# Optimization experiments

Measured on AMD Instinct MI355X. Metric: run time of the kernel, lower is better.

## Reference

```python
import jax, jax.numpy as jnp
import numpy as np

INPUT_SIZE = 512
HIDDEN_SIZE = 1024
SEQ_LEN = 512
BATCH = 64


def _xavier(key, shape):
    fan_out, fan_in = shape
    limit = float(np.sqrt(6.0 / (fan_in + fan_out)))
    return jax.random.uniform(key, shape, jnp.float32, -limit, limit)


def setup_inputs() -> dict:
    key = jax.random.key(0)
    ks = jax.random.split(key, 10)
    return {
        "x_seq": jax.random.normal(ks[0], (SEQ_LEN, BATCH, INPUT_SIZE), jnp.float32),
        "h": jax.random.normal(ks[1], (BATCH, HIDDEN_SIZE), jnp.float32),
        "U_c": _xavier(ks[2], (HIDDEN_SIZE, INPUT_SIZE)),
        "w_c": jax.random.normal(ks[3], (HIDDEN_SIZE,), jnp.float32),
        "b_c": jax.random.normal(ks[4], (HIDDEN_SIZE,), jnp.float32),
        "U_a": _xavier(ks[5], (HIDDEN_SIZE, INPUT_SIZE)),
        "w_a": jax.random.normal(ks[6], (HIDDEN_SIZE,), jnp.float32),
        "b_a": jax.random.normal(ks[7], (HIDDEN_SIZE,), jnp.float32),
        "U_h": _xavier(ks[8], (HIDDEN_SIZE, INPUT_SIZE)),
        "b_h": jax.random.normal(ks[9], (HIDDEN_SIZE,), jnp.float32),
    }


def reference(x_seq, h, U_c, w_c, b_c, U_a, w_a, b_a, U_h, b_h):
    # Precompute all input projections in one big batched GEMM each:
    # (S, B, I) @ (I, H) -> (S, B, H)
    xc = jnp.einsum("sbi,hi->sbh", x_seq, U_c) + b_c
    xa = jnp.einsum("sbi,hi->sbh", x_seq, U_a) + b_a
    xh = jnp.einsum("sbi,hi->sbh", x_seq, U_h) + b_h

    def step(h, proj):
        pc, pa, ph = proj
        c = jax.nn.sigmoid(pc + w_c * h)
        a = 1.0 + jnp.tanh(pa + w_a * h)
        h_new = c * h + (1.0 - c) * jnp.tanh(ph + a * h)
        return h_new, h_new

    hn, y_seq = jax.lax.scan(step, h, (xc, xa, xh))
    return y_seq, hn
```

## Files before the change

### kernel.cpp

```cpp
#include <hip/hip_runtime.h>
#include <hip/hip_bf16.h>
#include <stdint.h>

#define SEQLEN 512
#define NBATCH 64
#define KDIM   512
#define HDIM   1024
#define MTOT   (SEQLEN * NBATCH)
#define NTOT   (3 * HDIM)
#define STRIDE (NBATCH * HDIM)

typedef __attribute__((ext_vector_type(4))) float f32x4;
typedef _Float16 f16x8 __attribute__((ext_vector_type(8)));

__global__ __launch_bounds__(256) void cvt_x(const float* __restrict__ x,
                                             _Float16* __restrict__ xh,
                                             _Float16* __restrict__ xl) {
    int i = blockIdx.x * 256 + threadIdx.x;
    const float4* s = (const float4*)(x + (size_t)i * 8);
    float4 a = s[0], b = s[1];
    float v[8] = {a.x, a.y, a.z, a.w, b.x, b.y, b.z, b.w};
    f16x8 hi, lo;
#pragma unroll
    for (int j = 0; j < 8; ++j) {
        _Float16 h = (_Float16)v[j];
        hi[j] = h;
        lo[j] = (_Float16)(v[j] - (float)h);
    }
    *(f16x8*)(xh + (size_t)i * 8) = hi;
    *(f16x8*)(xl + (size_t)i * 8) = lo;
}

__global__ __launch_bounds__(256) void cvt_u(const float* __restrict__ Uc,
                                             const float* __restrict__ Ua,
                                             const float* __restrict__ Uh,
                                             _Float16* __restrict__ uh,
                                             _Float16* __restrict__ ul) {
    int i = blockIdx.x * 256 + threadIdx.x;
    int n = i >> 6;
    int kb = (i & 63) * 8;
    const float* src = (n < HDIM) ? (Uc + (size_t)n * KDIM)
                     : (n < 2 * HDIM) ? (Ua + (size_t)(n - HDIM) * KDIM)
                     : (Uh + (size_t)(n - 2 * HDIM) * KDIM);
    const float4* s = (const float4*)(src + kb);
    float4 a = s[0], b = s[1];
    float v[8] = {a.x, a.y, a.z, a.w, b.x, b.y, b.z, b.w};
    f16x8 hi, lo;
#pragma unroll
    for (int j = 0; j < 8; ++j) {
        _Float16 h = (_Float16)v[j];
        hi[j] = h;
        lo[j] = (_Float16)(v[j] - (float)h);
    }
    *(f16x8*)(uh + (size_t)n * KDIM + kb) = hi;
    *(f16x8*)(ul + (size_t)n * KDIM + kb) = lo;
}

#define BM 256
#define BN 256
#define BK 32
#define NT_N (NTOT / BN)
#define GRID ((MTOT / BM) * NT_N)
#define KT_N (KDIM / BK)

__device__ __forceinline__ void gload16(const _Float16* g, _Float16* l) {
    __builtin_amdgcn_global_load_lds((const __attribute__((address_space(1))) void*)g,
                                     (__attribute__((address_space(3))) void*)l,
                                     16, 0, 0);
}

__device__ __forceinline__ f32x4 mfma16(f16x8 a, f16x8 b, f32x4 c) {
    return __builtin_amdgcn_mfma_f32_16x16x32_f16(a, b, c, 0, 0, 0);
}

__global__ __launch_bounds__(512, 2) void gemm_f16x2(const _Float16* __restrict__ Ah,
                                                     const _Float16* __restrict__ Al,
                                                     const _Float16* __restrict__ Bh,
                                                     const _Float16* __restrict__ Bl,
                                                     float* __restrict__ pc,
                                                     float* __restrict__ pa,
                                                     float* __restrict__ ph) {
    __shared__ _Float16 lds[2][4][BM * BK];

    int bid  = blockIdx.x;
    int bm   = bid / NT_N;
    int bn   = bid % NT_N;
    int tid  = threadIdx.x;
    int lane = tid & 63;
    int wave = tid >> 6;
    int wr   = wave >> 2;
    int wc   = wave & 3;

    size_t row_off = (size_t)(tid >> 2) * KDIM
                   + (size_t)(((tid & 3) ^ ((tid >> 3) & 3)) * 8);
    const _Float16* gAh = Ah + (size_t)bm * BM * KDIM + row_off;
    const _Float16* gAl = Al + (size_t)bm * BM * KDIM + row_off;
    const _Float16* gBh = Bh + (size_t)bn * BN * KDIM + row_off;
    const _Float16* gBl = Bl + (size_t)bn * BN * KDIM + row_off;
    const size_t HPAN = (size_t)128 * KDIM;
    int t8 = tid * 8;

#define SPAIR(buf, plane, gp, kt) do { int _g = (kt) * BK;                     \
    gload16((gp) + _g,        &lds[buf][plane][t8]);                           \
    gload16((gp) + HPAN + _g, &lds[buf][plane][t8 + 4096]); } while (0)

    f32x4 acc[8][4];
#pragma unroll
    for (int i = 0; i < 8; ++i)
#pragma unroll
        for (int j = 0; j < 4; ++j)
            acc[i][j] = (f32x4){0.f, 0.f, 0.f, 0.f};

    int ro = lane & 15;
    int ko = ((lane >> 4) ^ ((lane >> 1) & 3)) * 8;

    f16x8 a_[4][2], b_[4][2];

#define READ_A(mh) _Pragma("unroll")                                           \
    for (int i = 0; i < 4; ++i) {                                              \
        int row = wr * 128 + ((mh) * 4 + i) * 16 + ro;                         \
        a_[i][0] = *(const f16x8*)(&lds[cur][0][row * BK + ko]);               \
        a_[i][1] = *(const f16x8*)(&lds[cur][1][row * BK + ko]);               \
    }
#define READ_B() _Pragma("unroll")                                             \
    for (int j = 0; j < 4; ++j) {                                              \
        int row = wc * 64 + j * 16 + ro;                                       \
        b_[j][0] = *(const f16x8*)(&lds[cur][2][row * BK + ko]);               \
        b_[j][1] = *(const f16x8*)(&lds[cur][3][row * BK + ko]);               \
    }
#define MFMA_HALF(mh) _Pragma("unroll")                                        \
    for (int i = 0; i < 4; ++i) _Pragma("unroll")                              \
        for (int j = 0; j < 4; ++j) {                                          \
            f32x4 c = acc[(mh) * 4 + i][j];                                    \
            c = mfma16(a_[i][0], b_[j][1], c);                      \
            c = mfma16(a_[i][1], b_[j][0], c);                      \
            c = mfma16(a_[i][0], b_[j][0], c);                      \
            acc[(mh) * 4 + i][j] = c;                                          \
        }

    SPAIR(0, 0, gAh, 0);
    SPAIR(0, 1, gAl, 0);
    SPAIR(0, 2, gBh, 0);
    SPAIR(0, 3, gBl, 0);

    for (int kt = 0; kt < KT_N; ++kt) {
        int cur = kt & 1, nxt = 1 - cur;
        bool pre = (kt < KT_N - 1);
        __builtin_amdgcn_sched_barrier(0);
        asm volatile("s_waitcnt vmcnt(0)" ::: "memory");
        __builtin_amdgcn_s_barrier();
        __builtin_amdgcn_sched_barrier(0);

        READ_B();
        READ_A(0);
        if (pre) { SPAIR(nxt, 0, gAh, kt + 1); SPAIR(nxt, 1, gAl, kt + 1); }
        __builtin_amdgcn_s_setprio(1);
        MFMA_HALF(0);
        __builtin_amdgcn_s_setprio(0);
        READ_A(1);
        if (pre) { SPAIR(nxt, 2, gBh, kt + 1); SPAIR(nxt, 3, gBl, kt + 1); }
        __builtin_amdgcn_s_setprio(1);
        MFMA_HALF(1);
        __builtin_amdgcn_s_setprio(0);
    }

    int n0 = bn * BN;
    float* outp; int nb;
    if (n0 < HDIM)            { outp = pc; nb = n0; }
    else if (n0 < 2 * HDIM)   { outp = pa; nb = n0 - HDIM; }
    else                      { outp = ph; nb = n0 - 2 * HDIM; }

#pragma unroll
    for (int ai = 0; ai < 8; ++ai)
#pragma unroll
        for (int bj = 0; bj < 4; ++bj) {
            int m = bm * BM + wr * 128 + ai * 16 + (lane >> 4) * 4;
            int n = nb + wc * 64 + bj * 16 + (lane & 15);
#pragma unroll
            for (int r = 0; r < 4; ++r)
                outp[(size_t)(m + r) * HDIM + n] = acc[ai][bj][r];
        }
#undef SPAIR
#undef READ_A
#undef READ_B
#undef MFMA_HALF
}

__global__ __launch_bounds__(256) void recur(const float* __restrict__ pc_a,
                                             const float* __restrict__ pa_a,
                                             float* out,
                                             const float* __restrict__ h0,
                                             const float* __restrict__ wc_,
                                             const float* __restrict__ bc_,
                                             const float* __restrict__ wa_,
                                             const float* __restrict__ ba_,
                                             const float* __restrict__ bh_) {
    int idx = blockIdx.x * 256 + threadIdx.x;
    int j = idx & (HDIM - 1);
    float h  = h0[idx];
    float wc = wc_[j], bc = bc_[j];
    float wa = wa_[j], ba = ba_[j];
    float bh = bh_[j];

#define PF 32
    float pc[PF], pa[PF], ph[PF];
#pragma unroll
    for (int u = 0; u < PF; ++u) {
        pc[u] = pc_a[(size_t)u * STRIDE + idx];
        pa[u] = pa_a[(size_t)u * STRIDE + idx];
        ph[u] = out [(size_t)u * STRIDE + idx];
    }

    for (int sb = 0; sb < SEQLEN; sb += PF) {
#pragma unroll
        for (int u = 0; u < PF; ++u) {
            int s = sb + u;
            float vc = pc[u], va = pa[u], vh = ph[u];
            int sp = s + PF; sp = (sp < SEQLEN) ? sp : (SEQLEN - 1);
            pc[u] = pc_a[(size_t)sp * STRIDE + idx];
            pa[u] = pa_a[(size_t)sp * STRIDE + idx];
            ph[u] = out [(size_t)sp * STRIDE + idx];

            float zc = (vc + bc) + wc * h;
            float za = (va + ba) + wa * h;
            float c  = 1.0f / (1.0f + expf(-zc));
            float a  = 1.0f + tanhf(za);
            float ht = tanhf((vh + bh) + a * h);
            h = c * h + (1.0f - c) * ht;
            out[(size_t)s * STRIDE + idx] = h;
        }
    }
    out[(size_t)SEQLEN * STRIDE + idx] = h;
}

extern "C" void kernel_launch(void* const* d_in, const int* in_sizes, int n_in,
                              void* d_out, int out_size, void* d_ws, size_t ws_size,
                              hipStream_t stream) {
    const float* x_seq = (const float*)d_in[0];
    const float* h0    = (const float*)d_in[1];
    const float* U_c   = (const float*)d_in[2];
    const float* w_c   = (const float*)d_in[3];
    const float* b_c   = (const float*)d_in[4];
    const float* U_a   = (const float*)d_in[5];
    const float* w_a   = (const float*)d_in[6];
    const float* b_a   = (const float*)d_in[7];
    const float* U_h   = (const float*)d_in[8];
    const float* b_h   = (const float*)d_in[9];
    float* out = (float*)d_out;

    char* ws = (char*)d_ws;
    const size_t MB = 1024 * 1024;
    float*    ws_pc = (float*)ws;
    float*    ws_pa = (float*)(ws + 128 * MB);
    _Float16* x_hi  = (_Float16*)(ws + 256 * MB);
    _Float16* x_lo  = (_Float16*)(ws + 288 * MB);
    _Float16* u_hi  = (_Float16*)(ws + 320 * MB);
    _Float16* u_lo  = (_Float16*)(ws + 323 * MB);

    cvt_x<<<dim3(MTOT * KDIM / 8 / 256), dim3(256), 0, stream>>>(x_seq, x_hi, x_lo);
    cvt_u<<<dim3(NTOT * KDIM / 8 / 256), dim3(256), 0, stream>>>(U_c, U_a, U_h, u_hi, u_lo);
    gemm_f16x2<<<dim3(GRID), dim3(512), 0, stream>>>(
        x_hi, x_lo, u_hi, u_lo, ws_pc, ws_pa, out);
    recur<<<dim3(STRIDE / 256), dim3(256), 0, stream>>>(ws_pc, ws_pa, out, h0,
                                                        w_c, b_c, w_a, b_a, b_h);
}
```

Before: 462.7 us.

## Deepen GEMM LDS pipeline to prefetch two tiles ahead with one barrier

```diff
diff --git a/kernel.cpp b/kernel.cpp
--- a/kernel.cpp
+++ b/kernel.cpp
@@ -103,6 +103,9 @@
 #define SPAIR(buf, plane, gp, kt) do { int _g = (kt) * BK;                     \
     gload16((gp) + _g,        &lds[buf][plane][t8]);                           \
     gload16((gp) + HPAN + _g, &lds[buf][plane][t8 + 4096]); } while (0)
+#define STAGE4(buf, kt) do {                                                   \
+    SPAIR(buf, 0, gAh, kt); SPAIR(buf, 1, gAl, kt);                            \
+    SPAIR(buf, 2, gBh, kt); SPAIR(buf, 3, gBl, kt); } while (0)
 
     f32x4 acc[8][4];
 #pragma unroll
@@ -114,54 +117,56 @@
     int ro = lane & 15;
     int ko = ((lane >> 4) ^ ((lane >> 1) & 3)) * 8;
 
-    f16x8 a_[4][2], b_[4][2];
-
-#define READ_A(mh) _Pragma("unroll")                                           \
+    f16x8 a0_[4][2], a1_[4][2], b_[4][2];
+
+#define READ_AH(arr, buf, mh) _Pragma("unroll")                                \
     for (int i = 0; i < 4; ++i) {                                              \
         int row = wr * 128 + ((mh) * 4 + i) * 16 + ro;                         \
-        a_[i][0] = *(const f16x8*)(&lds[cur][0][row * BK + ko]);               \
-        a_[i][1] = *(const f16x8*)(&lds[cur][1][row * BK + ko]);               \
-    }
-#define READ_B() _Pragma("unroll")                                             \
+        arr[i][0] = *(const f16x8*)(&lds[buf][0][row * BK + ko]);              \
+        arr[i][1] = *(const f16x8*)(&lds[buf][1][row * BK + ko]);              \
+    }
+#define READ_BB(buf) _Pragma("unroll")                                         \
     for (int j = 0; j < 4; ++j) {                                              \
         int row = wc * 64 + j * 16 + ro;                                       \
-        b_[j][0] = *(const f16x8*)(&lds[cur][2][row * BK + ko]);               \
-        b_[j][1] = *(const f16x8*)(&lds[cur][3][row * BK + ko]);               \
-    }
-#define MFMA_HALF(mh) _Pragma("unroll")                                        \
+        b_[j][0] = *(const f16x8*)(&lds[buf][2][row * BK + ko]);               \
+        b_[j][1] = *(const f16x8*)(&lds[buf][3][row * BK + ko]);               \
+    }
+#define MFMA_HALF(arr, mh) _Pragma("unroll")                                   \
     for (int i = 0; i < 4; ++i) _Pragma("unroll")                              \
         for (int j = 0; j < 4; ++j) {                                          \
             f32x4 c = acc[(mh) * 4 + i][j];                                    \
-            c = mfma16(a_[i][0], b_[j][1], c);                      \
-            c = mfma16(a_[i][1], b_[j][0], c);                      \
-            c = mfma16(a_[i][0], b_[j][0], c);                      \
+            c = mfma16(arr[i][0], b_[j][1], c);                     \
+            c = mfma16(arr[i][1], b_[j][0], c);                     \
+            c = mfma16(arr[i][0], b_[j][0], c);                     \
             acc[(mh) * 4 + i][j] = c;                                          \
         }
-
-    SPAIR(0, 0, gAh, 0);
-    SPAIR(0, 1, gAl, 0);
-    SPAIR(0, 2, gBh, 0);
-    SPAIR(0, 3, gBl, 0);
+#define BARRIER_PINNED do {                                                    \
+    __builtin_amdgcn_sched_barrier(0);                                         \
+    asm volatile("s_waitcnt vmcnt(0)" ::: "memory");                           \
+    __builtin_amdgcn_s_barrier();                                              \
+    __builtin_amdgcn_sched_barrier(0); } while (0)
+
+    STAGE4(0, 0);
+    BARRIER_PINNED;
+    READ_BB(0);
+    READ_AH(a0_, 0, 0);
+    STAGE4(1, 1);
 
     for (int kt = 0; kt < KT_N; ++kt) {
         int cur = kt & 1, nxt = 1 - cur;
-        bool pre = (kt < KT_N - 1);
-        __builtin_amdgcn_sched_barrier(0);
-        asm volatile("s_waitcnt vmcnt(0)" ::: "memory");
-        __builtin_amdgcn_s_barrier();
-        __builtin_amdgcn_sched_barrier(0);
-
-        READ_B();
-        READ_A(0);
-        if (pre) { SPAIR(nxt, 0, gAh, kt + 1); SPAIR(nxt, 1, gAl, kt + 1); }
+        READ_AH(a1_, cur, 1);
         __builtin_amdgcn_s_setprio(1);
-        MFMA_HALF(0);
+        MFMA_HALF(a0_, 0);
         __builtin_amdgcn_s_setprio(0);
-        READ_A(1);
-        if (pre) { SPAIR(nxt, 2, gBh, kt + 1); SPAIR(nxt, 3, gBl, kt + 1); }
         __builtin_amdgcn_s_setprio(1);
-        MFMA_HALF(1);
+        MFMA_HALF(a1_, 1);
         __builtin_amdgcn_s_setprio(0);
+        if (kt < KT_N - 1) {
+            BARRIER_PINNED;
+            READ_BB(nxt);
+            READ_AH(a0_, nxt, 0);
+            if (kt < KT_N - 2) STAGE4(cur, kt + 2);
+        }
     }
 
     int n0 = bn * BN;
@@ -181,9 +186,11 @@
                 outp[(size_t)(m + r) * HDIM + n] = acc[ai][bj][r];
         }
 #undef SPAIR
-#undef READ_A
-#undef READ_B
+#undef STAGE4
+#undef READ_AH
+#undef READ_BB
 #undef MFMA_HALF
+#undef BARRIER_PINNED
 }
 
 __global__ __launch_bounds__(256) void recur(const float* __restrict__ pc_a,
```

Result: faster. 453.3 us (-2.1%).

## Switch GEMM to 32x32x16 MFMA tiles and use fast sigmoid/tanh in recurrence

Applied to the files above, without the earlier changes.

```diff
diff --git a/kernel.cpp b/kernel.cpp
--- a/kernel.cpp
+++ b/kernel.cpp
@@ -10,7 +10,8 @@
 #define NTOT   (3 * HDIM)
 #define STRIDE (NBATCH * HDIM)
 
-typedef __attribute__((ext_vector_type(4))) float f32x4;
+typedef __attribute__((ext_vector_type(4)))  float f32x4;
+typedef __attribute__((ext_vector_type(16))) float f32x16;
 typedef _Float16 f16x8 __attribute__((ext_vector_type(8)));
 
 __global__ __launch_bounds__(256) void cvt_x(const float* __restrict__ x,
@@ -69,8 +70,8 @@
                                      16, 0, 0);
 }
 
-__device__ __forceinline__ f32x4 mfma16(f16x8 a, f16x8 b, f32x4 c) {
-    return __builtin_amdgcn_mfma_f32_16x16x32_f16(a, b, c, 0, 0, 0);
+__device__ __forceinline__ f32x16 mfma32(f16x8 a, f16x8 b, f32x16 c) {
+    return __builtin_amdgcn_mfma_f32_32x32x16_f16(a, b, c, 0, 0, 0);
 }
 
 __global__ __launch_bounds__(512, 2) void gemm_f16x2(const _Float16* __restrict__ Ah,
@@ -104,44 +105,47 @@
     gload16((gp) + _g,        &lds[buf][plane][t8]);                           \
     gload16((gp) + HPAN + _g, &lds[buf][plane][t8 + 4096]); } while (0)
 
-    f32x4 acc[8][4];
-#pragma unroll
-    for (int i = 0; i < 8; ++i)
-#pragma unroll
-        for (int j = 0; j < 4; ++j)
-            acc[i][j] = (f32x4){0.f, 0.f, 0.f, 0.f};
-
-    int ro = lane & 15;
-    int ko = ((lane >> 4) ^ ((lane >> 1) & 3)) * 8;
-
-    f16x8 a_[4][2], b_[4][2];
-
-#define READ_A(mh) _Pragma("unroll")                                           \
+    f32x16 acc[4][2];
+#pragma unroll
+    for (int i = 0; i < 4; ++i)
+#pragma unroll
+        for (int j = 0; j < 2; ++j)
+#pragma unroll
+            for (int r = 0; r < 16; ++r)
+                acc[i][j][r] = 0.f;
+
+    int rr = lane & 31;
+    int kg = lane >> 5;
+    int kx = (lane >> 1) & 3;
+
+    f16x8 a_[4][2], b_[2][2];
+
+#define READ_A(ks) _Pragma("unroll")                                           \
     for (int i = 0; i < 4; ++i) {                                              \
-        int row = wr * 128 + ((mh) * 4 + i) * 16 + ro;                         \
+        int row = wr * 128 + i * 32 + rr;                                      \
+        int ko = ((((ks) * 2 + kg) ^ kx) * 8);                                 \
         a_[i][0] = *(const f16x8*)(&lds[cur][0][row * BK + ko]);               \
         a_[i][1] = *(const f16x8*)(&lds[cur][1][row * BK + ko]);               \
     }
-#define READ_B() _Pragma("unroll")                                             \
-    for (int j = 0; j < 4; ++j) {                                              \
-        int row = wc * 64 + j * 16 + ro;                                       \
+#define READ_B(ks) _Pragma("unroll")                                           \
+    for (int j = 0; j < 2; ++j) {                                              \
+        int row = wc * 64 + j * 32 + rr;                                       \
+        int ko = ((((ks) * 2 + kg) ^ kx) * 8);                                 \
         b_[j][0] = *(const f16x8*)(&lds[cur][2][row * BK + ko]);               \
         b_[j][1] = *(const f16x8*)(&lds[cur][3][row * BK + ko]);               \
     }
-#define MFMA_HALF(mh) _Pragma("unroll")                                        \
+#define MFMA_STEP() _Pragma("unroll")                                          \
     for (int i = 0; i < 4; ++i) _Pragma("unroll")                              \
-        for (int j = 0; j < 4; ++j) {                                          \
-            f32x4 c = acc[(mh) * 4 + i][j];                                    \
-            c = mfma16(a_[i][0], b_[j][1], c);                      \
-            c = mfma16(a_[i][1], b_[j][0], c);                      \
-            c = mfma16(a_[i][0], b_[j][0], c);                      \
-            acc[(mh) * 4 + i][j] = c;                                          \
+        for (int j = 0; j < 2; ++j) {                                          \
+            f32x16 c = acc[i][j];                                              \
+            c = mfma32(a_[i][0], b_[j][1], c);                      \
+            c = mfma32(a_[i][1], b_[j][0], c);                      \
+            c = mfma32(a_[i][0], b_[j][0], c);                      \
+            acc[i][j] = c;                                                     \
         }
 
-    SPAIR(0, 0, gAh, 0);
-    SPAIR(0, 1, gAl, 0);
-    SPAIR(0, 2, gBh, 0);
-    SPAIR(0, 3, gBl, 0);
+    SPAIR(0, 0, gAh, 0); SPAIR(0, 1, gAl, 0);
+    SPAIR(0, 2, gBh, 0); SPAIR(0, 3, gBl, 0);
 
     for (int kt = 0; kt < KT_N; ++kt) {
         int cur = kt & 1, nxt = 1 - cur;
@@ -151,16 +155,17 @@
         __builtin_amdgcn_s_barrier();
         __builtin_amdgcn_sched_barrier(0);
 
-        READ_B();
+        READ_B(0);
         READ_A(0);
         if (pre) { SPAIR(nxt, 0, gAh, kt + 1); SPAIR(nxt, 1, gAl, kt + 1); }
         __builtin_amdgcn_s_setprio(1);
-        MFMA_HALF(0);
+        MFMA_STEP();
         __builtin_amdgcn_s_setprio(0);
         READ_A(1);
+        READ_B(1);
         if (pre) { SPAIR(nxt, 2, gBh, kt + 1); SPAIR(nxt, 3, gBl, kt + 1); }
         __builtin_amdgcn_s_setprio(1);
-        MFMA_HALF(1);
+        MFMA_STEP();
         __builtin_amdgcn_s_setprio(0);
     }
 
@@ -171,19 +176,32 @@
     else                      { outp = ph; nb = n0 - 2 * HDIM; }
 
 #pragma unroll
-    for (int ai = 0; ai < 8; ++ai)
-#pragma unroll
-        for (int bj = 0; bj < 4; ++bj) {
-            int m = bm * BM + wr * 128 + ai * 16 + (lane >> 4) * 4;
-            int n = nb + wc * 64 + bj * 16 + (lane & 15);
-#pragma unroll
-            for (int r = 0; r < 4; ++r)
-                outp[(size_t)(m + r) * HDIM + n] = acc[ai][bj][r];
+    for (int i = 0; i < 4; ++i)
+#pragma unroll
+        for (int j = 0; j < 2; ++j) {
+            int mbase = bm * BM + wr * 128 + i * 32 + 4 * kg;
+            int nn = nb + wc * 64 + j * 32 + rr;
+#pragma unroll
+            for (int t = 0; t < 4; ++t)
+#pragma unroll
+                for (int q = 0; q < 4; ++q)
+                    outp[(size_t)(mbase + q + 8 * t) * HDIM + nn] = acc[i][j][t * 4 + q];
         }
 #undef SPAIR
 #undef READ_A
 #undef READ_B
-#undef MFMA_HALF
+#undef MFMA_STEP
+}
+
+__device__ __forceinline__ float fsigmoid(float z) {
+    float e = __expf(-z);
+    return __builtin_amdgcn_rcpf(1.0f + e);
+}
+__device__ __forceinline__ float ftanh(float x) {
+    float ax = fminf(fabsf(x), 10.0f);
+    float e  = __expf(-2.0f * ax);
+    float t  = (1.0f - e) * __builtin_amdgcn_rcpf(1.0f + e);
+    return copysignf(t, x);
 }
 
 __global__ __launch_bounds__(256) void recur(const float* __restrict__ pc_a,
@@ -223,9 +241,9 @@
 
             float zc = (vc + bc) + wc * h;
             float za = (va + ba) + wa * h;
-            float c  = 1.0f / (1.0f + expf(-zc));
-            float a  = 1.0f + tanhf(za);
-            float ht = tanhf((vh + bh) + a * h);
+            float c  = fsigmoid(zc);
+            float a  = 1.0f + ftanh(za);
+            float ht = ftanh((vh + bh) + a * h);
             h = c * h + (1.0f - c) * ht;
             out[(size_t)s * STRIDE + idx] = h;
         }
```

Result: slower. 494.2 us (+6.8%).

## Widen GEMM N-tile to 384 and reduce recurrence prefetch depth

Applied to the files above, without the earlier changes.

```diff
diff --git a/kernel.cpp b/kernel.cpp
--- a/kernel.cpp
+++ b/kernel.cpp
@@ -57,11 +57,16 @@
 }
 
 #define BM 256
-#define BN 256
+#define BN 384
 #define BK 32
 #define NT_N (NTOT / BN)
 #define GRID ((MTOT / BM) * NT_N)
 #define KT_N (KDIM / BK)
+#define OFF_AH 0
+#define OFF_AL 8192
+#define OFF_BH 16384
+#define OFF_BL 28672
+#define BUF_HW 40960
 
 __device__ __forceinline__ void gload16(const _Float16* g, _Float16* l) {
     __builtin_amdgcn_global_load_lds((const __attribute__((address_space(1))) void*)g,
@@ -80,7 +85,7 @@
                                                      float* __restrict__ pc,
                                                      float* __restrict__ pa,
                                                      float* __restrict__ ph) {
-    __shared__ _Float16 lds[2][4][BM * BK];
+    __shared__ _Float16 lds[2][BUF_HW];
 
     int bid  = blockIdx.x;
     int bm   = bid / NT_N;
@@ -97,51 +102,53 @@
     const _Float16* gAl = Al + (size_t)bm * BM * KDIM + row_off;
     const _Float16* gBh = Bh + (size_t)bn * BN * KDIM + row_off;
     const _Float16* gBl = Bl + (size_t)bn * BN * KDIM + row_off;
-    const size_t HPAN = (size_t)128 * KDIM;
+    const size_t P128 = (size_t)128 * KDIM;
     int t8 = tid * 8;
 
-#define SPAIR(buf, plane, gp, kt) do { int _g = (kt) * BK;                     \
-    gload16((gp) + _g,        &lds[buf][plane][t8]);                           \
-    gload16((gp) + HPAN + _g, &lds[buf][plane][t8 + 4096]); } while (0)
-
-    f32x4 acc[8][4];
+#define SA(buf, off, gp, kt) do { int _g = (kt) * BK;                          \
+    gload16((gp) + _g,            &lds[buf][(off) + t8]);                      \
+    gload16((gp) + P128 + _g,     &lds[buf][(off) + 4096 + t8]); } while (0)
+#define SB(buf, off, gp, kt) do { int _g = (kt) * BK;                          \
+    gload16((gp) + _g,            &lds[buf][(off) + t8]);                      \
+    gload16((gp) + P128 + _g,     &lds[buf][(off) + 4096 + t8]);               \
+    gload16((gp) + 2 * P128 + _g, &lds[buf][(off) + 8192 + t8]); } while (0)
+
+    f32x4 acc[8][6];
 #pragma unroll
     for (int i = 0; i < 8; ++i)
 #pragma unroll
-        for (int j = 0; j < 4; ++j)
+        for (int j = 0; j < 6; ++j)
             acc[i][j] = (f32x4){0.f, 0.f, 0.f, 0.f};
 
     int ro = lane & 15;
     int ko = ((lane >> 4) ^ ((lane >> 1) & 3)) * 8;
 
-    f16x8 a_[4][2], b_[4][2];
-
-#define READ_A(mh) _Pragma("unroll")                                           \
+    f16x8 a0_[4][2], a1_[4][2], b_[6][2];
+
+#define READ_A(arr, mh) _Pragma("unroll")                                      \
     for (int i = 0; i < 4; ++i) {                                              \
         int row = wr * 128 + ((mh) * 4 + i) * 16 + ro;                         \
-        a_[i][0] = *(const f16x8*)(&lds[cur][0][row * BK + ko]);               \
-        a_[i][1] = *(const f16x8*)(&lds[cur][1][row * BK + ko]);               \
+        arr[i][0] = *(const f16x8*)(&lds[cur][OFF_AH + row * BK + ko]);        \
+        arr[i][1] = *(const f16x8*)(&lds[cur][OFF_AL + row * BK + ko]);        \
     }
 #define READ_B() _Pragma("unroll")                                             \
-    for (int j = 0; j < 4; ++j) {                                              \
-        int row = wc * 64 + j * 16 + ro;                                       \
-        b_[j][0] = *(const f16x8*)(&lds[cur][2][row * BK + ko]);               \
-        b_[j][1] = *(const f16x8*)(&lds[cur][3][row * BK + ko]);               \
-    }
-#define MFMA_HALF(mh) _Pragma("unroll")                                        \
+    for (int j = 0; j < 6; ++j) {                                              \
+        int row = wc * 96 + j * 16 + ro;                                       \
+        b_[j][0] = *(const f16x8*)(&lds[cur][OFF_BH + row * BK + ko]);         \
+        b_[j][1] = *(const f16x8*)(&lds[cur][OFF_BL + row * BK + ko]);         \
+    }
+#define MFMA_HALF(arr, mh) _Pragma("unroll")                                   \
     for (int i = 0; i < 4; ++i) _Pragma("unroll")                              \
-        for (int j = 0; j < 4; ++j) {                                          \
+        for (int j = 0; j < 6; ++j) {                                          \
             f32x4 c = acc[(mh) * 4 + i][j];                                    \
-            c = mfma16(a_[i][0], b_[j][1], c);                      \
-            c = mfma16(a_[i][1], b_[j][0], c);                      \
-            c = mfma16(a_[i][0], b_[j][0], c);                      \
+            c = mfma16(arr[i][0], b_[j][1], c);                     \
+            c = mfma16(arr[i][1], b_[j][0], c);                     \
+            c = mfma16(arr[i][0], b_[j][0], c);                     \
             acc[(mh) * 4 + i][j] = c;                                          \
         }
 
-    SPAIR(0, 0, gAh, 0);
-    SPAIR(0, 1, gAl, 0);
-    SPAIR(0, 2, gBh, 0);
-    SPAIR(0, 3, gBl, 0);
+    SA(0, OFF_AH, gAh, 0); SA(0, OFF_AL, gAl, 0);
+    SB(0, OFF_BH, gBh, 0); SB(0, OFF_BL, gBl, 0);
 
     for (int kt = 0; kt < KT_N; ++kt) {
         int cur = kt & 1, nxt = 1 - cur;
@@ -152,35 +159,34 @@
         __builtin_amdgcn_sched_barrier(0);
 
         READ_B();
-        READ_A(0);
-        if (pre) { SPAIR(nxt, 0, gAh, kt + 1); SPAIR(nxt, 1, gAl, kt + 1); }
+        READ_A(a0_, 0);
+        if (pre) { SA(nxt, OFF_AH, gAh, kt + 1); SA(nxt, OFF_AL, gAl, kt + 1); }
         __builtin_amdgcn_s_setprio(1);
-        MFMA_HALF(0);
+        MFMA_HALF(a0_, 0);
         __builtin_amdgcn_s_setprio(0);
-        READ_A(1);
-        if (pre) { SPAIR(nxt, 2, gBh, kt + 1); SPAIR(nxt, 3, gBl, kt + 1); }
+        READ_A(a1_, 1);
+        if (pre) { SB(nxt, OFF_BH, gBh, kt + 1); SB(nxt, OFF_BL, gBl, kt + 1); }
         __builtin_amdgcn_s_setprio(1);
-        MFMA_HALF(1);
+        MFMA_HALF(a1_, 1);
         __builtin_amdgcn_s_setprio(0);
     }
 
-    int n0 = bn * BN;
-    float* outp; int nb;
-    if (n0 < HDIM)            { outp = pc; nb = n0; }
-    else if (n0 < 2 * HDIM)   { outp = pa; nb = n0 - HDIM; }
-    else                      { outp = ph; nb = n0 - 2 * HDIM; }
-
-#pragma unroll
-    for (int ai = 0; ai < 8; ++ai)
-#pragma unroll
-        for (int bj = 0; bj < 4; ++bj) {
+#pragma unroll
+    for (int j = 0; j < 6; ++j) {
+        int ntb = bn * BN + wc * 96 + j * 16;
+        float* outp = (ntb < HDIM) ? pc : (ntb < 2 * HDIM) ? pa : ph;
+        int nb = ntb & (HDIM - 1);
+        int n = nb + (lane & 15);
+#pragma unroll
+        for (int ai = 0; ai < 8; ++ai) {
             int m = bm * BM + wr * 128 + ai * 16 + (lane >> 4) * 4;
-            int n = nb + wc * 64 + bj * 16 + (lane & 15);
 #pragma unroll
             for (int r = 0; r < 4; ++r)
-                outp[(size_t)(m + r) * HDIM + n] = acc[ai][bj][r];
+                outp[(size_t)(m + r) * HDIM + n] = acc[ai][j][r];
         }
-#undef SPAIR
+    }
+#undef SA
+#undef SB
 #undef READ_A
 #undef READ_B
 #undef MFMA_HALF
@@ -202,7 +208,7 @@
     float wa = wa_[j], ba = ba_[j];
     float bh = bh_[j];
 
-#define PF 32
+#define PF 16
     float pc[PF], pa[PF], ph[PF];
 #pragma unroll
     for (int u = 0; u < PF; ++u) {
```

Result: slower. 730.8 us (+57.9%).
